# Kernel tuning notes

Hardware: AMD Instinct MI355X
Metric: run time of the kernel (lower is better)

## Reference

```python
import jax, jax.numpy as jnp
import numpy as np

V, I, H, OUT = 50000, 512, 1024, 2   # node_size, input_dim, hidden_dim, out_dim
P, L = 256, 64                       # num paths, max path length
NH = 32                              # num attention heads
HD = H // NH


def setup_inputs() -> dict:
    key = jax.random.key(0)
    ks = jax.random.split(key, 10)
    paths = jax.random.randint(ks[0], (P, L), 0, V)          # padded path token ids
    lengths = jax.random.randint(ks[1], (P,), 1, L + 1)       # true path lengths in [1, L]
    g = lambda k, shape, s: jax.random.normal(k, shape, jnp.float32) * s
    return {
        "paths": paths,
        "lengths": lengths,
        "emb_table": g(ks[2], (V, I), 0.1),
        "W_ih": g(ks[3], (4 * H, I), 0.02),
        "W_hh": g(ks[4], (4 * H, H), 0.02),
        "b_ih": jnp.zeros((4 * H,), jnp.float32),
        "b_hh": jnp.zeros((4 * H,), jnp.float32),
        "W_in": g(ks[5], (3 * H, H), 0.02),   # packed q,k,v in_proj (torch layout)
        "b_in": jnp.zeros((3 * H,), jnp.float32),
        "W_out": g(ks[6], (H, H), 0.02),
        "b_out": jnp.zeros((H,), jnp.float32),
        "W_lin": g(ks[7], (OUT, H), 0.02),
        "b_lin": jnp.zeros((OUT,), jnp.float32),
    }


def reference(paths, lengths, emb_table, W_ih, W_hh, b_ih, b_hh,
              W_in, b_in, W_out, b_out, W_lin, b_lin):
    p = paths.shape[0]
    x = emb_table[paths]                 # [P, L, I] (batched embedding of all ragged paths)
    xs = jnp.swapaxes(x, 0, 1)           # [L, P, I] time-major for scan
    b = b_ih + b_hh

    def step(carry, xt):                 # single-layer LSTM, torch gate order i,f,g,o
        h, c = carry
        gates = xt @ W_ih.T + h @ W_hh.T + b          # [P, 4H]
        i_g, f_g, g_g, o_g = jnp.split(gates, 4, axis=-1)
        c = jax.nn.sigmoid(f_g) * c + jax.nn.sigmoid(i_g) * jnp.tanh(g_g)
        h = jax.nn.sigmoid(o_g) * jnp.tanh(c)
        return (h, c), h

    h0 = jnp.zeros((p, H), x.dtype)
    _, hs = jax.lax.scan(step, (h0, h0), xs)          # [L, P, H]
    # final hidden of each path at its true length (equiv. to per-path h_n in the torch loop)
    final_h = hs[lengths - 1, jnp.arange(p)]          # [P, H]
    sum_hidden = final_h[None]                        # [1, P, H]  (seq=1, batch=P)

    # nn.MultiheadAttention(sum_hidden, sum_hidden, sum_hidden), seq_len = 1
    qkv = sum_hidden @ W_in.T + b_in                  # [1, P, 3H]
    q, k, v = jnp.split(qkv, 3, axis=-1)
    qh = q.reshape(1, p, NH, HD)
    kh = k.reshape(1, p, NH, HD)
    vh = v.reshape(1, p, NH, HD)
    scale = 1.0 / np.sqrt(HD).astype(np.float32)
    scores = jnp.einsum('qpnd,kpnd->pnqk', qh * scale, kh)   # [P, NH, 1, 1]
    attn = jax.nn.softmax(scores, axis=-1)
    ctx = jnp.einsum('pnqk,kpnd->qpnd', attn, vh).reshape(1, p, H)
    attn_out = ctx @ W_out.T + b_out                  # [1, P, H]

    # MaxPool2d((P,1)) on (C=1, H=P, W=hidden): max over the P paths
    pooled = jnp.max(attn_out, axis=1, keepdims=True)  # [1, 1, H]
    out = jax.nn.sigmoid(pooled @ W_lin.T + b_lin)     # [1, 1, OUT]
    return out
```

## Files before the change

kernel.cpp:

```cpp
#include <hip/hip_runtime.h>
#include <stdint.h>

typedef unsigned short u16;
typedef unsigned int u32;
typedef __attribute__((ext_vector_type(8))) short s16x8;
typedef __attribute__((ext_vector_type(4))) float f32x4;

#define P_ 256
#define L_ 64
#define IDIM 512
#define H_ 1024
#define PH (P_ * H_)

__device__ __forceinline__ u16 f2bf(float f){union{float f;u32 u;}v;v.f=f;u32 u=v.u;return (u16)((u+0x7FFFu+((u>>16)&1u))>>16);}
__device__ __forceinline__ float sigf(float x){return 1.0f/(1.0f+__expf(-x));}
__device__ __forceinline__ float tanhf_(float x){return 1.0f-2.0f/(__expf(2.0f*x)+1.0f);}

__device__ __forceinline__ s16x8 pack8v(float4 a, float4 b){
  s16x8 r;
  r[0]=(short)f2bf(a.x); r[1]=(short)f2bf(a.y); r[2]=(short)f2bf(a.z); r[3]=(short)f2bf(a.w);
  r[4]=(short)f2bf(b.x); r[5]=(short)f2bf(b.y); r[6]=(short)f2bf(b.z); r[7]=(short)f2bf(b.w);
  return r;
}
__device__ __forceinline__ s16x8 pack8(const float* s){
  return pack8v(*(const float4*)s, *(const float4*)(s+4));
}
__device__ __forceinline__ void st16_coh(u16* addr, s16x8 v){
  asm volatile("global_store_dwordx4 %0, %1, off sc0 sc1" :: "v"(addr), "v"(v) : "memory");
}
__device__ __forceinline__ void st_pair(u16* addr, float hv, int lane){
  u32 b = (u32)f2bf(hv);
  u32 other = __shfl_xor(b, 1);
  if ((lane & 1) == 0) {
    u32 w = b | (other << 16);
    __hip_atomic_store((u32*)addr, w, __ATOMIC_RELAXED, __HIP_MEMORY_SCOPE_AGENT);
  }
}
__device__ __forceinline__ void set_flag(u32* f, u32 v){
  __hip_atomic_store(f, v, __ATOMIC_RELAXED, __HIP_MEMORY_SCOPE_AGENT);
}
__device__ __forceinline__ void poll_flags(u32* fg, u32 target, int wid, int lane){
  if (wid == 0) {
    for (;;) {
      u32 f = __hip_atomic_load(&fg[lane], __ATOMIC_RELAXED, __HIP_MEMORY_SCOPE_AGENT);
      if (__all((int)(f >= target))) break;
      __builtin_amdgcn_s_sleep(1);
    }
  }
  asm volatile("" ::: "memory");
  __syncthreads();
}
__device__ __forceinline__ void poll_prod(u32* fg, u32 target, int wid, int lane){
  const int jbp = wid * 2 + (lane & 1) + 16 * ((lane >> 1) & 3);
  for (;;) {
    u32 f = __hip_atomic_load(&fg[jbp], __ATOMIC_RELAXED, __HIP_MEMORY_SCOPE_AGENT);
    if (__all((int)(f >= target))) break;
    __builtin_amdgcn_s_sleep(1);
  }
  asm volatile("" ::: "memory");
}
__device__ __forceinline__ void lds_barrier(){
  asm volatile("s_waitcnt lgkmcnt(0)" ::: "memory");
  __builtin_amdgcn_sched_barrier(0);
  __builtin_amdgcn_s_barrier();
  __builtin_amdgcn_sched_barrier(0);
}

__global__ void __launch_bounds__(512, 1)
tagger_net(const int* __restrict__ paths, const int* __restrict__ lengths,
           const float* __restrict__ emb,
           const float* __restrict__ Wih, const float* __restrict__ Whh,
           const float* __restrict__ bih, const float* __restrict__ bhh,
           const float* __restrict__ Win, const float* __restrict__ bin,
           const float* __restrict__ Wout, const float* __restrict__ bout,
           const float* __restrict__ Wlin, const float* __restrict__ blin,
           u16* __restrict__ X, u16* __restrict__ Hbuf,
           u16* __restrict__ vbuf, float* __restrict__ pmax,
           u32* flags, float* __restrict__ out)
{
  __shared__ __align__(16) float S[16384];
  const int tid  = threadIdx.x;
  const int wid  = tid >> 6, lane = tid & 63;
  const int lrow = lane & 15, lgrp = lane >> 4;
  const int bid  = blockIdx.x;
  const int g = bid & 3, jb = bid >> 2;
  const int p0 = g * 64, j0 = jb * 16;
  u32* fgrp = flags + g * 64;
  u32* myflag = fgrp + jb;

  for (int it = 0; it < 8; ++it) {
    int e = (it * 512 + tid) * 8;
    int row = e >> 9, col = e & 511;
    int tok = paths[(p0 + row) * L_ + jb];
    const float* s = emb + (size_t)tok * IDIM + col;
    st16_coh(X + ((size_t)jb * P_ + p0 + row) * IDIM + col,
             pack8v(*(const float4*)s, *(const float4*)(s + 4)));
  }
  {
    int row = tid >> 3, cp = tid & 7;
    __hip_atomic_store((u32*)&Hbuf[(size_t)(p0 + row) * H_ + j0 + cp * 2], 0u,
                       __ATOMIC_RELAXED, __HIP_MEMORY_SCOPE_AGENT);
  }
  __syncthreads();
  if (tid == 0) set_flag(myflag, 1u);

  s16x8 breg[6][4];
#pragma unroll
  for (int i = 0; i < 6; ++i) {
    const int kg = (wid + 8 * i) * 32 + lgrp * 8;
#pragma unroll
    for (int fn = 0; fn < 4; ++fn) {
      const int n = fn * H_ + j0 + lrow;
      const float* src = (kg < IDIM) ? (Wih + (size_t)n * IDIM + kg)
                                     : (Whh + (size_t)n * H_ + (kg - IDIM));
      breg[i][fn] = pack8(src);
    }
  }

  const int prow = p0 + (wid & 3) * 16 + lgrp * 4;
  int lenr[4]; float biasv[4];
#pragma unroll
  for (int r2 = 0; r2 < 4; ++r2) lenr[r2] = lengths[prow + r2];
#pragma unroll
  for (int fn = 0; fn < 4; ++fn) {
    int n = fn * H_ + j0 + lrow;
    biasv[fn] = bih[n] + bhh[n];
  }
  float cst[4] = {0.f,0.f,0.f,0.f}, hst[4] = {0.f,0.f,0.f,0.f};

  poll_flags(fgrp, 1u, wid, lane);

  const size_t aX = (size_t)(p0 + lrow) * IDIM + lgrp * 8;
  const size_t aH = (size_t)(p0 + lrow) * H_   + lgrp * 8;

  s16x8 fx[2][4];
#define LOADX(T) do { \
    const u16* Xt_ = X + (size_t)(T) * (P_ * IDIM) + aX; \
    _Pragma("unroll") \
    for (int i_ = 0; i_ < 2; ++i_) { \
      const int k0_ = (wid + 8 * i_) * 32; \
      _Pragma("unroll") \
      for (int fm_ = 0; fm_ < 4; ++fm_) \
        fx[i_][fm_] = *(const s16x8*)(Xt_ + (size_t)fm_ * (16 * IDIM) + k0_); \
    } } while (0)

  LOADX(0);

  for (int t = 0; t < L_; ++t) {
    const u16* Hr = Hbuf + (size_t)t * PH;
    u16*       Hw = Hbuf + (size_t)(t + 1) * PH;

    f32x4 acc[4][4];
#pragma unroll
    for (int a = 0; a < 4; ++a)
#pragma unroll
      for (int b = 0; b < 4; ++b)
#pragma unroll
        for (int e = 0; e < 4; ++e) acc[a][b][e] = 0.0f;

#pragma unroll
    for (int i = 0; i < 2; ++i)
#pragma unroll
      for (int fm = 0; fm < 4; ++fm)
#pragma unroll
        for (int fn = 0; fn < 4; ++fn)
          acc[fm][fn] = __builtin_amdgcn_mfma_f32_16x16x32_bf16(fx[i][fm], breg[i][fn], acc[fm][fn], 0, 0, 0);

    poll_prod(fgrp, (u32)(t + 1), wid, lane);

    const u16* Hp = Hr + aH;
    s16x8 fhA[2][4], fhB[2][4];
#pragma unroll
    for (int i = 0; i < 2; ++i) {
      const int kh = wid * 32 + i * 256;
#pragma unroll
      for (int fm = 0; fm < 4; ++fm)
        fhA[i][fm] = *(const s16x8*)(Hp + (size_t)fm * (16 * H_) + kh);
    }
#pragma unroll
    for (int i = 0; i < 2; ++i) {
      const int kh = wid * 32 + 512 + i * 256;
#pragma unroll
      for (int fm = 0; fm < 4; ++fm)
        fhB[i][fm] = *(const s16x8*)(Hp + (size_t)fm * (16 * H_) + kh);
    }
#pragma unroll
    for (int i = 0; i < 2; ++i)
#pragma unroll
      for (int fm = 0; fm < 4; ++fm)
#pragma unroll
        for (int fn = 0; fn < 4; ++fn)
          acc[fm][fn] = __builtin_amdgcn_mfma_f32_16x16x32_bf16(fhA[i][fm], breg[2 + i][fn], acc[fm][fn], 0, 0, 0);
    { const int tp1 = (t < L_ - 1) ? (t + 1) : (L_ - 1); LOADX(tp1); }
#pragma unroll
    for (int i = 0; i < 2; ++i)
#pragma unroll
      for (int fm = 0; fm < 4; ++fm)
#pragma unroll
        for (int fn = 0; fn < 4; ++fn)
          acc[fm][fn] = __builtin_amdgcn_mfma_f32_16x16x32_bf16(fhB[i][fm], breg[4 + i][fn], acc[fm][fn], 0, 0, 0);

    f32x4 red[4];
#pragma unroll
    for (int rr = 0; rr < 2; ++rr) {
#pragma unroll
      for (int fm = 0; fm < 4; ++fm)
#pragma unroll
        for (int q = 0; q < 2; ++q)
          *(f32x4*)&S[(wid * 8 + fm * 2 + q) * 256 + lane * 4] = acc[fm][2 * rr + q];
      lds_barrier();
      if (wid < 4) {
#pragma unroll
        for (int q = 0; q < 2; ++q) {
          f32x4 v = *(const f32x4*)&S[(wid * 2 + q) * 256 + lane * 4];
#pragma unroll
          for (int s = 1; s < 8; ++s)
            v += *(const f32x4*)&S[(s * 8 + wid * 2 + q) * 256 + lane * 4];
          red[2 * rr + q] = v;
        }
      }
      lds_barrier();
    }

    if (wid < 4) {
#pragma unroll
      for (int r2 = 0; r2 < 4; ++r2) {
        if (t < lenr[r2]) {
          float gi = red[0][r2] + biasv[0];
          float gf = red[1][r2] + biasv[1];
          float gg = red[2][r2] + biasv[2];
          float go = red[3][r2] + biasv[3];
          float cn = sigf(gf) * cst[r2] + sigf(gi) * tanhf_(gg);
          cst[r2] = cn;
          hst[r2] = sigf(go) * tanhf_(cn);
        }
        st_pair(&Hw[(size_t)(prow + r2) * H_ + j0 + lrow], hst[r2], lane);
      }
    }
    __syncthreads();
    if (tid == 0) set_flag(myflag, (u32)(t + 2));
  }

  const u16* hfin = Hbuf + (size_t)L_ * PH;
  poll_flags(fgrp, 65u, wid, lane);

  {
    f32x4 acc2[4];
#pragma unroll
    for (int a = 0; a < 4; ++a)
#pragma unroll
      for (int e = 0; e < 4; ++e) acc2[a][e] = 0.0f;
    const u16* hp = hfin + aH;
    const float* wv = Win + (size_t)(2 * H_ + j0 + lrow) * H_;
#pragma unroll
    for (int ic = 0; ic < 4; ++ic) {
      const int k0 = wid * 128 + ic * 32;
      s16x8 fbv = pack8(wv + k0 + lgrp * 8);
#pragma unroll
      for (int fm = 0; fm < 4; ++fm) {
        s16x8 fav = *(const s16x8*)(hp + (size_t)fm * (16 * H_) + k0);
        acc2[fm] = __builtin_amdgcn_mfma_f32_16x16x32_bf16(fav, fbv, acc2[fm], 0, 0, 0);
      }
    }
#pragma unroll
    for (int fm = 0; fm < 4; ++fm)
      *(f32x4*)&S[(wid * 4 + fm) * 256 + lane * 4] = acc2[fm];
    __syncthreads();
    if (wid < 4) {
      f32x4 rv = *(const f32x4*)&S[(wid) * 256 + lane * 4];
#pragma unroll
      for (int s = 1; s < 8; ++s)
        rv += *(const f32x4*)&S[(s * 4 + wid) * 256 + lane * 4];
      float bvj = bin[2 * H_ + j0 + lrow];
#pragma unroll
      for (int r2 = 0; r2 < 4; ++r2)
        st_pair(&vbuf[(size_t)(prow + r2) * H_ + j0 + lrow], rv[r2] + bvj, lane);
    }
  }
  __syncthreads();
  if (tid == 0) set_flag(myflag, 66u);
  poll_flags(fgrp, 66u, wid, lane);

  {
    f32x4 acc2[4];
#pragma unroll
    for (int a = 0; a < 4; ++a)
#pragma unroll
      for (int e = 0; e < 4; ++e) acc2[a][e] = 0.0f;
    const u16* vp = vbuf + aH;
    const float* wo = Wout + (size_t)(j0 + lrow) * H_;
#pragma unroll
    for (int ic = 0; ic < 4; ++ic) {
      const int k0 = wid * 128 + ic * 32;
      s16x8 fbv = pack8(wo + k0 + lgrp * 8);
#pragma unroll
      for (int fm = 0; fm < 4; ++fm) {
        s16x8 fav = *(const s16x8*)(vp + (size_t)fm * (16 * H_) + k0);
        acc2[fm] = __builtin_amdgcn_mfma_f32_16x16x32_bf16(fav, fbv, acc2[fm], 0, 0, 0);
      }
    }
#pragma unroll
    for (int fm = 0; fm < 4; ++fm)
      *(f32x4*)&S[(wid * 4 + fm) * 256 + lane * 4] = acc2[fm];
    __syncthreads();
    if (wid < 4) {
      f32x4 rv = *(const f32x4*)&S[(wid) * 256 + lane * 4];
#pragma unroll
      for (int s = 1; s < 8; ++s)
        rv += *(const f32x4*)&S[(s * 4 + wid) * 256 + lane * 4];
      float bo = bout[j0 + lrow];
      float m = fmaxf(fmaxf(rv[0], rv[1]), fmaxf(rv[2], rv[3])) + bo;
      __syncthreads();
      S[(wid * 4 + lgrp) * 16 + lrow] = m;
    } else {
      __syncthreads();
    }
    __syncthreads();
    if (tid < 16) {
      float mx = S[tid];
#pragma unroll
      for (int s2 = 1; s2 < 16; ++s2) mx = fmaxf(mx, S[s2 * 16 + tid]);
      __hip_atomic_store(&pmax[(size_t)g * H_ + j0 + tid], mx, __ATOMIC_RELAXED, __HIP_MEMORY_SCOPE_AGENT);
    }
  }
  __syncthreads();
  if (tid == 0) set_flag(myflag, 67u);

  if (bid != 0) return;

  if (wid == 0) {
    for (int g2 = 0; g2 < 4; ++g2) {
      for (;;) {
        u32 f = __hip_atomic_load(&flags[g2 * 64 + lane], __ATOMIC_RELAXED, __HIP_MEMORY_SCOPE_AGENT);
        if (__all((int)(f >= 67u))) break;
        __builtin_amdgcn_s_sleep(1);
      }
    }
  }
  asm volatile("" ::: "memory");
  __syncthreads();
  {
    int j2 = tid * 2;
    float s0 = 0.f, s1 = 0.f;
#pragma unroll
    for (int e = 0; e < 2; ++e) {
      float pv = pmax[j2 + e];
#pragma unroll
      for (int gg2 = 1; gg2 < 4; ++gg2) pv = fmaxf(pv, pmax[gg2 * H_ + j2 + e]);
      s0 += pv * Wlin[j2 + e];
      s1 += pv * Wlin[H_ + j2 + e];
    }
    S[tid] = s0; S[512 + tid] = s1;
    __syncthreads();
    for (int s2 = 256; s2 > 0; s2 >>= 1) {
      if (tid < s2) { S[tid] += S[tid + s2]; S[512 + tid] += S[512 + tid + s2]; }
      __syncthreads();
    }
    if (tid == 0) {
      out[0] = sigf(S[0] + blin[0]);
      out[1] = sigf(S[512] + blin[1]);
    }
  }
}

extern "C" void kernel_launch(void* const* d_in, const int* in_sizes, int n_in,
                              void* d_out, int out_size, void* d_ws, size_t ws_size,
                              hipStream_t stream) {
  const int*   paths   = (const int*)d_in[0];
  const int*   lengths = (const int*)d_in[1];
  const float* emb     = (const float*)d_in[2];
  const float* Wih     = (const float*)d_in[3];
  const float* Whh     = (const float*)d_in[4];
  const float* bih     = (const float*)d_in[5];
  const float* bhh     = (const float*)d_in[6];
  const float* Win     = (const float*)d_in[7];
  const float* bin     = (const float*)d_in[8];
  const float* Wout    = (const float*)d_in[9];
  const float* bout    = (const float*)d_in[10];
  const float* Wlin    = (const float*)d_in[11];
  const float* blin    = (const float*)d_in[12];
  float* out = (float*)d_out;

  char* ws = (char*)d_ws;
  u32*   flags  = (u32*)  (ws);
  float* pmax   = (float*)(ws + 4096);
  u16*   X      = (u16*)  (ws + 32768);
  u16*   Hbuf   = (u16*)  (ws + 16810240);
  u16*   vbuf   = (u16*)  (ws + 50888960);

  hipMemsetAsync(flags, 0, 1024, stream);
  tagger_net<<<256, 512, 0, stream>>>(paths, lengths, emb, Wih, Whh, bih, bhh,
                                      Win, bin, Wout, bout, Wlin, blin,
                                      X, Hbuf, vbuf, pmax, flags, out);
}
```

Before: 576.8 us.

## Use per-wave byte flags to drop end-of-step block barrier in LSTM

Each LSTM flag word now holds four bytes, one per producing wave. Each of the four writer waves stores its own progress byte after waiting for its h stores, so the block no longer needs a __syncthreads before signalling. Consumers check all bytes at once with a SWAR compare. Polling moves to wave 0 followed by a raw s_barrier, replacing the earlier scheme where every wave polled. This shortens the per-timestep critical path, at the cost of byte-granular coherence and SWAR logic that only holds while counters stay below 128.

```diff
diff --git a/kernel.cpp b/kernel.cpp
--- a/kernel.cpp
+++ b/kernel.cpp
@@ -36,28 +36,41 @@
     __hip_atomic_store((u32*)addr, w, __ATOMIC_RELAXED, __HIP_MEMORY_SCOPE_AGENT);
   }
 }
-__device__ __forceinline__ void set_flag(u32* f, u32 v){
-  __hip_atomic_store(f, v, __ATOMIC_RELAXED, __HIP_MEMORY_SCOPE_AGENT);
+__device__ __forceinline__ void set_flag_word(u32* f, u32 v){
+  __hip_atomic_store(f, v * 0x01010101u, __ATOMIC_RELAXED, __HIP_MEMORY_SCOPE_AGENT);
+}
+__device__ __forceinline__ void set_flag_byte(u32* f, int byte_idx, u32 v){
+  asm volatile("global_store_byte %0, %1, off sc0 sc1"
+               :: "v"((char*)f + byte_idx), "v"(v) : "memory");
+}
+__device__ __forceinline__ int bytes_ok(u32 f, u32 tt){
+  return (((f | 0x80808080u) - tt) & 0x80808080u) == 0x80808080u;
 }
 __device__ __forceinline__ void poll_flags(u32* fg, u32 target, int wid, int lane){
+  const u32 tt = target * 0x01010101u;
   if (wid == 0) {
     for (;;) {
       u32 f = __hip_atomic_load(&fg[lane], __ATOMIC_RELAXED, __HIP_MEMORY_SCOPE_AGENT);
-      if (__all((int)(f >= target))) break;
+      if (__all(bytes_ok(f, tt))) break;
       __builtin_amdgcn_s_sleep(1);
     }
   }
   asm volatile("" ::: "memory");
   __syncthreads();
 }
-__device__ __forceinline__ void poll_prod(u32* fg, u32 target, int wid, int lane){
-  const int jbp = wid * 2 + (lane & 1) + 16 * ((lane >> 1) & 3);
-  for (;;) {
-    u32 f = __hip_atomic_load(&fg[jbp], __ATOMIC_RELAXED, __HIP_MEMORY_SCOPE_AGENT);
-    if (__all((int)(f >= target))) break;
-    __builtin_amdgcn_s_sleep(1);
+__device__ __forceinline__ void poll_flags_fast(u32* fg, u32 target, int wid, int lane){
+  const u32 tt = target * 0x01010101u;
+  if (wid == 0) {
+    for (;;) {
+      u32 f = __hip_atomic_load(&fg[lane], __ATOMIC_RELAXED, __HIP_MEMORY_SCOPE_AGENT);
+      if (__all(bytes_ok(f, tt))) break;
+      __builtin_amdgcn_s_sleep(1);
+    }
   }
   asm volatile("" ::: "memory");
+  __builtin_amdgcn_sched_barrier(0);
+  __builtin_amdgcn_s_barrier();
+  __builtin_amdgcn_sched_barrier(0);
 }
 __device__ __forceinline__ void lds_barrier(){
   asm volatile("s_waitcnt lgkmcnt(0)" ::: "memory");
@@ -102,7 +115,7 @@
                        __ATOMIC_RELAXED, __HIP_MEMORY_SCOPE_AGENT);
   }
   __syncthreads();
-  if (tid == 0) set_flag(myflag, 1u);
+  if (tid == 0) set_flag_word(myflag, 1u);
 
   s16x8 breg[6][4];
 #pragma unroll
@@ -166,7 +179,7 @@
         for (int fn = 0; fn < 4; ++fn)
           acc[fm][fn] = __builtin_amdgcn_mfma_f32_16x16x32_bf16(fx[i][fm], breg[i][fn], acc[fm][fn], 0, 0, 0);
 
-    poll_prod(fgrp, (u32)(t + 1), wid, lane);
+    poll_flags_fast(fgrp, (u32)(t + 1), wid, lane);
 
     const u16* Hp = Hr + aH;
     s16x8 fhA[2][4], fhB[2][4];
@@ -236,9 +249,9 @@
         }
         st_pair(&Hw[(size_t)(prow + r2) * H_ + j0 + lrow], hst[r2], lane);
       }
-    }
-    __syncthreads();
-    if (tid == 0) set_flag(myflag, (u32)(t + 2));
+      asm volatile("s_waitcnt vmcnt(0)" ::: "memory");
+      if (lane == 0) set_flag_byte(myflag, wid, (u32)(t + 2));
+    }
   }
 
   const u16* hfin = Hbuf + (size_t)L_ * PH;
@@ -278,7 +291,7 @@
     }
   }
   __syncthreads();
-  if (tid == 0) set_flag(myflag, 66u);
+  if (tid == 0) set_flag_word(myflag, 66u);
   poll_flags(fgrp, 66u, wid, lane);
 
   {
@@ -324,15 +337,16 @@
     }
   }
   __syncthreads();
-  if (tid == 0) set_flag(myflag, 67u);
+  if (tid == 0) set_flag_word(myflag, 67u);
 
   if (bid != 0) return;
 
   if (wid == 0) {
+    const u32 tt = 67u * 0x01010101u;
     for (int g2 = 0; g2 < 4; ++g2) {
       for (;;) {
         u32 f = __hip_atomic_load(&flags[g2 * 64 + lane], __ATOMIC_RELAXED, __HIP_MEMORY_SCOPE_AGENT);
-        if (__all((int)(f >= 67u))) break;
+        if (__all(bytes_ok(f, tt))) break;
         __builtin_amdgcn_s_sleep(1);
       }
     }
```

New measurement: 828.4 us. +43.6%, slower.
